# Kernel optimization log

Hardware: AMD Instinct MI355X
Metric: run time of the kernel (lower is better)

Reference implementation:

```python
import jax, jax.numpy as jnp
import numpy as np

B, S, DIN, DOUT = 4, 2048, 4096, 4096
W_SCALE = 64.0   # makes round(weight*scale) produce non-trivial int8 values
X_SCALE = 16.0   # input_scale so x*scale truncates to non-zero int32 values


def setup_inputs() -> dict:
    key = jax.random.key(0)
    k1, k2, k3 = jax.random.split(key, 3)
    # kaiming_uniform fan_in: bound = sqrt(6/fan_in)
    bound = float(np.sqrt(6.0 / DIN))
    weight = jax.random.uniform(k1, (DOUT, DIN), jnp.float32, -bound, bound)
    x = jax.random.normal(k2, (B, S, DIN), jnp.float32)
    bias = jax.random.normal(k3, (DOUT,), jnp.float32) * 0.01
    weight_scale = jnp.full((DOUT,), W_SCALE, jnp.float32)
    input_scale = jnp.full((1,), X_SCALE, jnp.float32)
    return {"x": x, "weight": weight, "bias": bias,
            "weight_scale": weight_scale, "input_scale": input_scale}


def reference(x, weight, bias, weight_scale, input_scale):
    # x = x * input_scale (pre-scale path of forward)
    xs = x * input_scale
    # fake-quant weights: round to int8 with wraparound, like torch .to(int8)
    w_int = jnp.round(weight * weight_scale[:, None]).astype(jnp.int8)
    # x.to(torch.int32): truncation toward zero
    x_int = xs.astype(jnp.int32)
    # F.linear on the integer-valued tensors (computed in f32: values are exact ints)
    acc = jnp.einsum('bsd,od->bso', x_int.astype(jnp.float32),
                     w_int.astype(jnp.float32))
    acc = acc + bias  # bias added inside linear
    # dequant: divide by per-channel weight_scale and the scalar input_scale
    out = acc / (weight_scale * input_scale)
    return out
```

## Files before the change

kernel.cpp:

```cpp
#include <hip/hip_runtime.h>

#define GM 8192
#define GN 4096
#define GK 4096

#define BM 128
#define BN 256
#define BK 64
#define NT (GK / BK)
#define ATILE (BM * BK)
#define TILE_LDS (BM * BK + BN * BK)

using int4v = __attribute__((ext_vector_type(4))) int;

__global__ __launch_bounds__(256) void quant_xw_k(
    const float4* __restrict__ x, unsigned int* __restrict__ xq,
    const float4* __restrict__ w, unsigned int* __restrict__ wq,
    const float* __restrict__ wscale, const float* __restrict__ iscale,
    int n4x, int n4tot) {
    const float xs = *iscale;
    const int stride = gridDim.x * blockDim.x;
    for (int i = blockIdx.x * blockDim.x + threadIdx.x; i < n4tot; i += stride) {
        if (i < n4x) {
            float4 v = x[i];
            int q0 = (int)(v.x * xs);
            int q1 = (int)(v.y * xs);
            int q2 = (int)(v.z * xs);
            int q3 = (int)(v.w * xs);
            xq[i] = (unsigned int)(q0 & 0xff)
                  | ((unsigned int)(q1 & 0xff) << 8)
                  | ((unsigned int)(q2 & 0xff) << 16)
                  | ((unsigned int)(q3 & 0xff) << 24);
        } else {
            int j = i - n4x;
            float s = wscale[j >> 10];
            float4 v = w[j];
            int q0 = (int)rintf(v.x * s);
            int q1 = (int)rintf(v.y * s);
            int q2 = (int)rintf(v.z * s);
            int q3 = (int)rintf(v.w * s);
            wq[j] = (unsigned int)(q0 & 0xff)
                  | ((unsigned int)(q1 & 0xff) << 8)
                  | ((unsigned int)(q2 & 0xff) << 16)
                  | ((unsigned int)(q3 & 0xff) << 24);
        }
    }
}

__global__ __launch_bounds__(256, 2) void qlinear_gemm_i8(
    const signed char* __restrict__ Aq,
    const signed char* __restrict__ Bq,
    const float* __restrict__ bias,
    const float* __restrict__ wscale,
    const float* __restrict__ iscale,
    float* __restrict__ C) {
    __shared__ signed char smem[3][TILE_LDS];

    const int tid  = threadIdx.x;
    const int wave = tid >> 6;
    const int lane = tid & 63;
    const int m0 = blockIdx.x * BM;
    const int n0 = blockIdx.y * BN;
    const int wm = (wave >> 1) * 64;
    const int wn = (wave & 1) * 128;

    int4v acc[4][8];
#pragma unroll
    for (int i = 0; i < 4; ++i)
#pragma unroll
        for (int j = 0; j < 8; ++j)
            acc[i][j] = int4v{0, 0, 0, 0};

    const int kcl = (((lane & 3) ^ ((lane >> 3) & 3))) * 16;
    const int segA = wave * 2;
    const signed char* gA0 = Aq + (size_t)(m0 + segA * 16 + (lane >> 2)) * GK + kcl;
    const int aoff = segA * 1024 + lane * 16;
    const int segB = wave * 4;
    const signed char* gB0 = Bq + (size_t)(n0 + segB * 16 + (lane >> 2)) * GK + kcl;
    const int boff = ATILE + segB * 1024 + lane * 16;

    const int pos = ((lane >> 4) ^ ((lane >> 1) & 3)) * 16;
    const int fAoff = (wm + (lane & 15)) * BK + pos;
    const int fBoff = ATILE + (wn + (lane & 15)) * BK + pos;

#define GLL16(g, l)                                                     \
    __builtin_amdgcn_global_load_lds(                                   \
        (__attribute__((address_space(1))) void*)(void*)(g),            \
        (__attribute__((address_space(3))) void*)(void*)(l), 16, 0, 0)

#define STAGE(kb, sb)                                                   \
    do {                                                                \
        GLL16(gA0 + (size_t)(kb), (sb) + aoff);                         \
        GLL16(gA0 + (size_t)16 * GK + (kb), (sb) + aoff + 1024);        \
        GLL16(gB0 + (size_t)(kb), (sb) + boff);                         \
        GLL16(gB0 + (size_t)16 * GK + (kb), (sb) + boff + 1024);        \
        GLL16(gB0 + (size_t)32 * GK + (kb), (sb) + boff + 2048);        \
        GLL16(gB0 + (size_t)48 * GK + (kb), (sb) + boff + 3072);        \
    } while (0)

    STAGE(0, smem[0]);
    STAGE(BK, smem[1]);
    asm volatile("s_waitcnt vmcnt(6)" ::: "memory");
    __builtin_amdgcn_s_barrier();
    __builtin_amdgcn_sched_barrier(0);

    int cur = 0;
    int kstage = 2 * BK;
    for (int t = 0; t < NT; ++t) {
        int nb = cur + 2; if (nb >= 3) nb -= 3;
        STAGE(kstage, smem[nb]);
        kstage += BK; if (kstage >= GK) kstage = 0;
        __builtin_amdgcn_sched_barrier(0);

        const signed char* sb = smem[cur];
        int4v a[4], b[8];
#pragma unroll
        for (int i = 0; i < 4; ++i)
            a[i] = *(const int4v*)(sb + fAoff + i * 16 * BK);
#pragma unroll
        for (int j = 0; j < 8; ++j)
            b[j] = *(const int4v*)(sb + fBoff + j * 16 * BK);

        __builtin_amdgcn_s_setprio(1);
#pragma unroll
        for (int mi = 0; mi < 4; ++mi)
#pragma unroll
            for (int ni = 0; ni < 8; ++ni)
                acc[mi][ni] = __builtin_amdgcn_mfma_i32_16x16x64_i8(
                    a[mi], b[ni], acc[mi][ni], 0, 0, 0);
        __builtin_amdgcn_s_setprio(0);

        asm volatile("s_waitcnt vmcnt(6)" ::: "memory");
        __builtin_amdgcn_s_barrier();
        __builtin_amdgcn_sched_barrier(0);
        cur += 1; if (cur == 3) cur = 0;
    }

    const float isc = *iscale;
#pragma unroll
    for (int ni = 0; ni < 8; ++ni) {
        const int col = n0 + wn + ni * 16 + (lane & 15);
        const float bs = bias[col];
        const float inv = 1.0f / (wscale[col] * isc);
#pragma unroll
        for (int mi = 0; mi < 4; ++mi) {
            const int row0 = m0 + wm + mi * 16 + (lane >> 4) * 4;
#pragma unroll
            for (int r = 0; r < 4; ++r) {
                C[(size_t)(row0 + r) * GN + col] =
                    ((float)acc[mi][ni][r] + bs) * inv;
            }
        }
    }
#undef STAGE
#undef GLL16
}

extern "C" void kernel_launch(void* const* d_in, const int* in_sizes, int n_in,
                              void* d_out, int out_size, void* d_ws, size_t ws_size,
                              hipStream_t stream) {
    const float* x      = (const float*)d_in[0];
    const float* w      = (const float*)d_in[1];
    const float* bias   = (const float*)d_in[2];
    const float* wscale = (const float*)d_in[3];
    const float* iscale = (const float*)d_in[4];
    float* out = (float*)d_out;

    signed char* xq = (signed char*)d_ws;
    signed char* wq = xq + (size_t)GM * GK;

    const int n4x = GM * GK / 4;
    const int n4w = GN * GK / 4;
    quant_xw_k<<<3072, 256, 0, stream>>>((const float4*)x, (unsigned int*)xq,
                                         (const float4*)w, (unsigned int*)wq,
                                         wscale, iscale, n4x, n4x + n4w);

    dim3 grid(GM / BM, GN / BN);
    qlinear_gemm_i8<<<grid, 256, 0, stream>>>(xq, wq, bias, wscale, iscale, out);
}
```

Measured before the change: 400.6 us.

## Enlarge GEMM tile to 256x256 with 8 waves and split-phase staging

Doubles the block tile to 256x256 and runs 512 threads (8 waves), each owning a 128x64 sub-tile. The aim is more operand reuse per LDS byte and less global traffic per output. Each K-step is split into two MFMA phases, with the A and B global-to-LDS loads interleaved between them and extra barriers around each phase. LDS use grows to 3x32KB per block, which lowers occupancy. The added barriers may also cost synchronisation time.

```diff
diff --git a/kernel.cpp b/kernel.cpp
--- a/kernel.cpp
+++ b/kernel.cpp
@@ -4,11 +4,11 @@
 #define GN 4096
 #define GK 4096
 
-#define BM 128
+#define BM 256
 #define BN 256
 #define BK 64
-#define NT (GK / BK)
-#define ATILE (BM * BK)
+#define NTILE (GK / BK)
+#define ABYTES (BM * BK)
 #define TILE_LDS (BM * BK + BN * BK)
 
 using int4v = __attribute__((ext_vector_type(4))) int;
@@ -47,112 +47,135 @@
     }
 }
 
-__global__ __launch_bounds__(256, 2) void qlinear_gemm_i8(
+__global__ __launch_bounds__(512, 2) void qlinear_gemm_i8(
     const signed char* __restrict__ Aq,
     const signed char* __restrict__ Bq,
     const float* __restrict__ bias,
     const float* __restrict__ wscale,
     const float* __restrict__ iscale,
     float* __restrict__ C) {
-    __shared__ signed char smem[3][TILE_LDS];
+    __shared__ signed char smem[3 * TILE_LDS];
 
     const int tid  = threadIdx.x;
     const int wave = tid >> 6;
     const int lane = tid & 63;
     const int m0 = blockIdx.x * BM;
     const int n0 = blockIdx.y * BN;
-    const int wm = (wave >> 1) * 64;
-    const int wn = (wave & 1) * 128;
-
-    int4v acc[4][8];
-#pragma unroll
-    for (int i = 0; i < 4; ++i)
-#pragma unroll
-        for (int j = 0; j < 8; ++j)
+    const int wm = (wave >> 2) * 128;
+    const int wn = (wave & 3) * 64;
+
+    int4v acc[8][4];
+#pragma unroll
+    for (int i = 0; i < 8; ++i)
+#pragma unroll
+        for (int j = 0; j < 4; ++j)
             acc[i][j] = int4v{0, 0, 0, 0};
 
-    const int kcl = (((lane & 3) ^ ((lane >> 3) & 3))) * 16;
-    const int segA = wave * 2;
-    const signed char* gA0 = Aq + (size_t)(m0 + segA * 16 + (lane >> 2)) * GK + kcl;
-    const int aoff = segA * 1024 + lane * 16;
-    const int segB = wave * 4;
-    const signed char* gB0 = Bq + (size_t)(n0 + segB * 16 + (lane >> 2)) * GK + kcl;
-    const int boff = ATILE + segB * 1024 + lane * 16;
-
-    const int pos = ((lane >> 4) ^ ((lane >> 1) & 3)) * 16;
-    const int fAoff = (wm + (lane & 15)) * BK + pos;
-    const int fBoff = ATILE + (wn + (lane & 15)) * BK + pos;
+    const int kc = ((tid & 3) ^ ((tid >> 3) & 3)) * 16;
+    const signed char* gA = Aq + (size_t)(m0 + (tid >> 2)) * GK + kc;
+    const signed char* gB = Bq + (size_t)(n0 + (tid >> 2)) * GK + kc;
+    const int dst = tid * 16;
+
+    const int pos = (((lane >> 4) ^ ((lane >> 1) & 3))) * 16;
+    const int fAo = (wm + (lane & 15)) * BK + pos;
+    const int fBo = ABYTES + (wn + (lane & 15)) * BK + pos;
 
 #define GLL16(g, l)                                                     \
     __builtin_amdgcn_global_load_lds(                                   \
         (__attribute__((address_space(1))) void*)(void*)(g),            \
         (__attribute__((address_space(3))) void*)(void*)(l), 16, 0, 0)
 
-#define STAGE(kb, sb)                                                   \
+#define STAGE_A(kb, soff)                                               \
     do {                                                                \
-        GLL16(gA0 + (size_t)(kb), (sb) + aoff);                         \
-        GLL16(gA0 + (size_t)16 * GK + (kb), (sb) + aoff + 1024);        \
-        GLL16(gB0 + (size_t)(kb), (sb) + boff);                         \
-        GLL16(gB0 + (size_t)16 * GK + (kb), (sb) + boff + 1024);        \
-        GLL16(gB0 + (size_t)32 * GK + (kb), (sb) + boff + 2048);        \
-        GLL16(gB0 + (size_t)48 * GK + (kb), (sb) + boff + 3072);        \
+        GLL16(gA + (kb), smem + (soff) + dst);                          \
+        GLL16(gA + (size_t)128 * GK + (kb), smem + (soff) + 8192 + dst);\
     } while (0)
-
-    STAGE(0, smem[0]);
-    STAGE(BK, smem[1]);
-    asm volatile("s_waitcnt vmcnt(6)" ::: "memory");
+#define STAGE_B(kb, soff)                                               \
+    do {                                                                \
+        GLL16(gB + (kb), smem + (soff) + ABYTES + dst);                 \
+        GLL16(gB + (size_t)128 * GK + (kb),                             \
+              smem + (soff) + ABYTES + 8192 + dst);                     \
+    } while (0)
+
+    STAGE_A(0, 0);
+    STAGE_B(0, 0);
+    STAGE_A(BK, TILE_LDS);
+    STAGE_B(BK, TILE_LDS);
+    asm volatile("s_waitcnt vmcnt(4)" ::: "memory");
     __builtin_amdgcn_s_barrier();
     __builtin_amdgcn_sched_barrier(0);
 
-    int cur = 0;
-    int kstage = 2 * BK;
-    for (int t = 0; t < NT; ++t) {
-        int nb = cur + 2; if (nb >= 3) nb -= 3;
-        STAGE(kstage, smem[nb]);
-        kstage += BK; if (kstage >= GK) kstage = 0;
-        __builtin_amdgcn_sched_barrier(0);
-
-        const signed char* sb = smem[cur];
-        int4v a[4], b[8];
-#pragma unroll
-        for (int i = 0; i < 4; ++i)
-            a[i] = *(const int4v*)(sb + fAoff + i * 16 * BK);
-#pragma unroll
-        for (int j = 0; j < 8; ++j)
-            b[j] = *(const int4v*)(sb + fBoff + j * 16 * BK);
-
+    int bc = 0;
+    int bn2 = TILE_LDS;
+    int bs = 2 * TILE_LDS;
+    int kst = 2 * BK;
+    for (int t = 0; t < NTILE; ++t) {
+        const signed char* fA = smem + bc + fAo;
+        const signed char* fB = smem + bc + fBo;
+        int4v aF[4], bF[4], aG[4];
+
+#pragma unroll
+        for (int i = 0; i < 4; ++i)
+            aF[i] = *(const int4v*)(fA + i * 1024);
+#pragma unroll
+        for (int j = 0; j < 4; ++j)
+            bF[j] = *(const int4v*)(fB + j * 1024);
+        STAGE_A(kst, bs);
+        __builtin_amdgcn_s_barrier();
+        asm volatile("s_waitcnt lgkmcnt(0)" ::: "memory");
+        __builtin_amdgcn_sched_barrier(0);
         __builtin_amdgcn_s_setprio(1);
 #pragma unroll
-        for (int mi = 0; mi < 4; ++mi)
-#pragma unroll
-            for (int ni = 0; ni < 8; ++ni)
-                acc[mi][ni] = __builtin_amdgcn_mfma_i32_16x16x64_i8(
-                    a[mi], b[ni], acc[mi][ni], 0, 0, 0);
+        for (int i = 0; i < 4; ++i)
+#pragma unroll
+            for (int j = 0; j < 4; ++j)
+                acc[i][j] = __builtin_amdgcn_mfma_i32_16x16x64_i8(
+                    aF[i], bF[j], acc[i][j], 0, 0, 0);
         __builtin_amdgcn_s_setprio(0);
-
-        asm volatile("s_waitcnt vmcnt(6)" ::: "memory");
-        __builtin_amdgcn_s_barrier();
-        __builtin_amdgcn_sched_barrier(0);
-        cur += 1; if (cur == 3) cur = 0;
+        __builtin_amdgcn_s_barrier();
+        __builtin_amdgcn_sched_barrier(0);
+
+#pragma unroll
+        for (int i = 0; i < 4; ++i)
+            aG[i] = *(const int4v*)(fA + (i + 4) * 1024);
+        STAGE_B(kst, bs);
+        __builtin_amdgcn_s_barrier();
+        asm volatile("s_waitcnt lgkmcnt(0)" ::: "memory");
+        __builtin_amdgcn_sched_barrier(0);
+        __builtin_amdgcn_s_setprio(1);
+#pragma unroll
+        for (int i = 0; i < 4; ++i)
+#pragma unroll
+            for (int j = 0; j < 4; ++j)
+                acc[i + 4][j] = __builtin_amdgcn_mfma_i32_16x16x64_i8(
+                    aG[i], bF[j], acc[i + 4][j], 0, 0, 0);
+        __builtin_amdgcn_s_setprio(0);
+        asm volatile("s_waitcnt vmcnt(4)" ::: "memory");
+        __builtin_amdgcn_s_barrier();
+        __builtin_amdgcn_sched_barrier(0);
+
+        int tmp = bc; bc = bn2; bn2 = bs; bs = tmp;
+        kst += BK; if (kst >= GK) kst = 0;
     }
 
     const float isc = *iscale;
 #pragma unroll
-    for (int ni = 0; ni < 8; ++ni) {
+    for (int ni = 0; ni < 4; ++ni) {
         const int col = n0 + wn + ni * 16 + (lane & 15);
-        const float bs = bias[col];
+        const float bs_ = bias[col];
         const float inv = 1.0f / (wscale[col] * isc);
 #pragma unroll
-        for (int mi = 0; mi < 4; ++mi) {
+        for (int mi = 0; mi < 8; ++mi) {
             const int row0 = m0 + wm + mi * 16 + (lane >> 4) * 4;
 #pragma unroll
             for (int r = 0; r < 4; ++r) {
                 C[(size_t)(row0 + r) * GN + col] =
-                    ((float)acc[mi][ni][r] + bs) * inv;
+                    ((float)acc[mi][ni][r] + bs_) * inv;
             }
         }
     }
-#undef STAGE
+#undef STAGE_A
+#undef STAGE_B
 #undef GLL16
 }
 
@@ -176,5 +199,5 @@
                                          wscale, iscale, n4x, n4x + n4w);
 
     dim3 grid(GM / BM, GN / BN);
-    qlinear_gemm_i8<<<grid, 256, 0, stream>>>(xq, wq, bias, wscale, iscale, out);
+    qlinear_gemm_i8<<<grid, 512, 0, stream>>>(xq, wq, bias, wscale, iscale, out);
 }
```

New measurement: 399.6 us. Within noise of the previous version (-0.2%).
